# Optimization experiments

Hardware: AMD Instinct MI355X
Metric: run time of the kernel (lower is better)

Reference implementation:

```python
import jax, jax.numpy as jnp
import numpy as np

N = 2_000_000
LAYER_DIMS = [6, 128, 48, 48, 48, 48, 48, 128, 3]  # 8 Linear layers


def setup_inputs() -> dict:
    key = jax.random.key(0)
    ks = jax.random.split(key, 2 + 2 * (len(LAYER_DIMS) - 1))
    inp = {
        "dimensions": jax.random.normal(ks[0], (N, 3), dtype=jnp.float32),
        "xyz": jax.random.normal(ks[1], (N, 3), dtype=jnp.float32),
    }
    # Kaiming-uniform-ish init like torch.nn.Linear defaults
    for i in range(len(LAYER_DIMS) - 1):
        fan_in, fan_out = LAYER_DIMS[i], LAYER_DIMS[i + 1]
        bound = 1.0 / np.sqrt(fan_in)
        inp[f"W{i+1}"] = jax.random.uniform(ks[2 + 2 * i], (fan_in, fan_out),
                                             minval=-bound, maxval=bound, dtype=jnp.float32)
        inp[f"b{i+1}"] = jax.random.uniform(ks[3 + 2 * i], (fan_out,),
                                             minval=-bound, maxval=bound, dtype=jnp.float32)
    return inp


def reference(dimensions, xyz,
              W1, b1, W2, b2, W3, b3, W4, b4,
              W5, b5, W6, b6, W7, b7, W8, b8) -> jnp.ndarray:
    x = jnp.concatenate([dimensions, xyz], axis=1)  # [N, 6]
    Ws = (W1, W2, W3, W4, W5, W6, W7)
    bs = (b1, b2, b3, b4, b5, b6, b7)
    for W, b in zip(Ws, bs):
        x = jax.nn.silu(x @ W + b)
    # final layer: Linear(128, 3) with Identity activation
    return x @ W8 + b8  # [N, 3]
```

## Files before the change

kernel.cpp:

```cpp
#include <hip/hip_runtime.h>

typedef __bf16 bf16x4 __attribute__((ext_vector_type(4)));
typedef short  s16x4  __attribute__((ext_vector_type(4)));
typedef float  f32x4  __attribute__((ext_vector_type(4)));

#define DEVFN static __device__ __forceinline__
#define BLOCK 512
#define NWAVES 8

DEVFN f32x4 mfma16(bf16x4 a, bf16x4 b, f32x4 c) {
  s16x4 as = __builtin_bit_cast(s16x4, a);
  s16x4 bs = __builtin_bit_cast(s16x4, b);
  return __builtin_amdgcn_mfma_f32_16x16x16bf16_1k(as, bs, c, 0, 0, 0);
}

DEVFN float silu_scaled(float y) {
  float e = __builtin_amdgcn_exp2f(-y);
  return y * __builtin_amdgcn_rcpf(1.0f + e);
}

DEVFN bf16x4 pksilu(f32x4 t) {
  bf16x4 r;
#pragma unroll
  for (int j = 0; j < 4; ++j) r[j] = (__bf16)silu_scaled(t[j]);
  return r;
}

DEVFN void sbar() { __builtin_amdgcn_sched_barrier(0x7F); }

#define OFF_W1   0u
#define OFF_W2   4096u
#define OFF_W3   16384u
#define OFF_W4   20992u
#define OFF_W5   25600u
#define OFF_W6   30208u
#define OFF_W7   34816u
#define OFF_BIAS 47104u
#define SMEM_TOTAL 49152u

#define LOG2E 1.44269504f
#define LN2   0.69314718f

DEVFN void packW(unsigned char* smem, unsigned base, const float* W, int K, int N, int tid) {
  int NT = N >> 4;
  int total = (K >> 4) * NT * 256;
  for (int t = tid; t < total; t += BLOCK) {
    int i = t & 3, ln = (t >> 2) & 63, f = t >> 8;
    int ks = f / NT, nt = f - ks * NT;
    int k = 16 * ks + 4 * (ln >> 4) + i;
    int n = 16 * nt + (ln & 15);
    *(__bf16*)(smem + base + (unsigned)f * 512u + (unsigned)ln * 8u + (unsigned)i * 2u)
        = (__bf16)W[k * N + n];
  }
}

DEVFN f32x4 ldb(const float* sB, int off, int nt, int g) {
  return *(const f32x4*)(sB + off + nt * 16 + 4 * g);
}

DEVFN bf16x4 ldw(const unsigned char* smem, unsigned addr) {
  return *(const bf16x4*)(smem + addr);
}

DEVFN void layer33(const unsigned char* smem, unsigned wbase, const float* sB, int bOffL,
                   unsigned wOff, int g, const bf16x4 (&xin)[2][3], bf16x4 (&xout)[2][3]) {
  f32x4 acc[2][3];
#pragma unroll
  for (int nt = 0; nt < 3; ++nt) {
    f32x4 bi = ldb(sB, bOffL, nt, g);
    acc[0][nt] = bi; acc[1][nt] = bi;
  }
#pragma unroll
  for (int ks = 0; ks < 3; ++ks)
#pragma unroll
    for (int nt = 0; nt < 3; ++nt) {
      bf16x4 w = ldw(smem, wbase + (unsigned)(ks * 3 + nt) * 512u + wOff);
      acc[0][nt] = mfma16(w, xin[0][ks], acc[0][nt]);
      acc[1][nt] = mfma16(w, xin[1][ks], acc[1][nt]);
    }
#pragma unroll
  for (int nt = 0; nt < 3; ++nt) {
    xout[0][nt] = pksilu(acc[0][nt]);
    xout[1][nt] = pksilu(acc[1][nt]);
  }
}

DEVFN void loadIn6(const float* __restrict__ dims, const float* __restrict__ xyz,
                   int grp, int g, int m, int N, float (&buf)[2][4]) {
#pragma unroll
  for (int rt = 0; rt < 2; ++rt) { buf[rt][0] = buf[rt][1] = buf[rt][2] = buf[rt][3] = 0.f; }
  if (g == 0) {
#pragma unroll
    for (int rt = 0; rt < 2; ++rt) {
      int row = grp * 32 + rt * 16 + m;
      if (row < N) {
        const float* dp = dims + (size_t)row * 3u;
        buf[rt][0] = dp[0]; buf[rt][1] = dp[1]; buf[rt][2] = dp[2];
        buf[rt][3] = xyz[(size_t)row * 3u];
      }
    }
  } else if (g == 1) {
#pragma unroll
    for (int rt = 0; rt < 2; ++rt) {
      int row = grp * 32 + rt * 16 + m;
      if (row < N) {
        const float* xp = xyz + (size_t)row * 3u;
        buf[rt][0] = xp[1]; buf[rt][1] = xp[2];
      }
    }
  }
}

__global__ void __launch_bounds__(BLOCK, 3)
pinn_mlp_kernel(const float* __restrict__ dims, const float* __restrict__ xyz,
                const float* __restrict__ W1, const float* __restrict__ b1,
                const float* __restrict__ W2, const float* __restrict__ b2,
                const float* __restrict__ W3, const float* __restrict__ b3,
                const float* __restrict__ W4, const float* __restrict__ b4,
                const float* __restrict__ W5, const float* __restrict__ b5,
                const float* __restrict__ W6, const float* __restrict__ b6,
                const float* __restrict__ W7, const float* __restrict__ b7,
                const float* __restrict__ W8, const float* __restrict__ b8,
                float* __restrict__ out, int N) {
  __shared__ __align__(16) unsigned char smem[SMEM_TOTAL];
  const int tid  = threadIdx.x;
  const int lane = tid & 63;
  const int wave = tid >> 6;
  const int m    = lane & 15;
  const int g    = lane >> 4;

  for (int t = tid; t < 2048; t += BLOCK) {
    int i = t & 3, ln = (t >> 2) & 63, nt = t >> 8;
    int k = 4 * (ln >> 4) + i;
    int n = 16 * nt + (ln & 15);
    float v = (k < 6) ? W1[k * 128 + n] * LOG2E : 0.f;
    *(__bf16*)(smem + OFF_W1 + (unsigned)nt * 512u + (unsigned)ln * 8u + (unsigned)i * 2u) = (__bf16)v;
  }
  packW(smem, OFF_W2, W2, 128, 48, tid);
  packW(smem, OFF_W3, W3, 48, 48, tid);
  packW(smem, OFF_W4, W4, 48, 48, tid);
  packW(smem, OFF_W5, W5, 48, 48, tid);
  packW(smem, OFF_W6, W6, 48, 48, tid);
  packW(smem, OFF_W7, W7, 48, 128, tid);
  float* sBw = (float*)(smem + OFF_BIAS);
  for (int t = tid; t < 512; t += BLOCK) {
    float v;
    if      (t < 128) v = b1[t] * LOG2E;
    else if (t < 176) v = b2[t - 128] * LOG2E;
    else if (t < 224) v = b3[t - 176] * LOG2E;
    else if (t < 272) v = b4[t - 224] * LOG2E;
    else if (t < 320) v = b5[t - 272] * LOG2E;
    else if (t < 368) v = b6[t - 320] * LOG2E;
    else if (t < 496) v = b7[t - 368] * LOG2E;
    else if (t < 499) v = b8[t - 496];
    else              v = 0.f;
    sBw[t] = v;
  }

  bf16x4 w8f[8];
#pragma unroll
  for (int ks = 0; ks < 8; ++ks) {
    w8f[ks][0] = (__bf16)0.f; w8f[ks][1] = (__bf16)0.f;
    w8f[ks][2] = (__bf16)0.f; w8f[ks][3] = (__bf16)0.f;
    if (m < 3) {
#pragma unroll
      for (int i = 0; i < 4; ++i) {
        int k = 16 * ks + 4 * g + i;
        w8f[ks][i] = (__bf16)(W8[k * 3 + m] * LN2);
      }
    }
  }

  __syncthreads();

  const float* sB = (const float*)(smem + OFF_BIAS);
  const unsigned wOff = (unsigned)lane * 8u;

  const int nGroups  = (N + 31) >> 5;
  const int gw0      = blockIdx.x * NWAVES + wave;
  const int gwStride = gridDim.x * NWAVES;

  float inC[2][4], inN[2][4];
  loadIn6(dims, xyz, gw0, g, m, N, inC);

  for (int grp = gw0; grp < nGroups; grp += gwStride) {
    const int base = grp * 32;

    bf16x4 x1[2];
#pragma unroll
    for (int rt = 0; rt < 2; ++rt)
#pragma unroll
      for (int j = 0; j < 4; ++j) x1[rt][j] = (__bf16)inC[rt][j];
    loadIn6(dims, xyz, grp + gwStride, g, m, N, inN);
    sbar();

    f32x4 acc2[2][3];
#pragma unroll
    for (int nt = 0; nt < 3; ++nt) {
      f32x4 bi = ldb(sB, 128, nt, g);
      acc2[0][nt] = bi; acc2[1][nt] = bi;
    }
#pragma unroll
    for (int p = 0; p < 4; ++p) {
      bf16x4 y[2][2];
#pragma unroll
      for (int c = 0; c < 2; ++c) {
        int nt = 2 * p + c;
        f32x4 bi = ldb(sB, 0, nt, g);
        bf16x4 w = ldw(smem, OFF_W1 + (unsigned)nt * 512u + wOff);
        y[0][c] = pksilu(mfma16(w, x1[0], bi));
        y[1][c] = pksilu(mfma16(w, x1[1], bi));
      }
      sbar();
#pragma unroll
      for (int c = 0; c < 2; ++c) {
        int ks = 2 * p + c;
#pragma unroll
        for (int nt = 0; nt < 3; ++nt) {
          bf16x4 w = ldw(smem, OFF_W2 + (unsigned)(ks * 3 + nt) * 512u + wOff);
          acc2[0][nt] = mfma16(w, y[0][c], acc2[0][nt]);
          acc2[1][nt] = mfma16(w, y[1][c], acc2[1][nt]);
        }
      }
      sbar();
    }
    bf16x4 xa[2][3], xb[2][3];
#pragma unroll
    for (int nt = 0; nt < 3; ++nt) {
      xa[0][nt] = pksilu(acc2[0][nt]);
      xa[1][nt] = pksilu(acc2[1][nt]);
    }
    sbar();

    layer33(smem, OFF_W3, sB, 176, wOff, g, xa, xb); sbar();
    layer33(smem, OFF_W4, sB, 224, wOff, g, xb, xa); sbar();
    layer33(smem, OFF_W5, sB, 272, wOff, g, xa, xb); sbar();
    layer33(smem, OFF_W6, sB, 320, wOff, g, xb, xa); sbar();

    f32x4 acc8[2];
    {
      f32x4 bi8 = ldb(sB, 496, 0, g);
      acc8[0] = bi8; acc8[1] = bi8;
    }
#pragma unroll
    for (int p = 0; p < 4; ++p) {
      f32x4 a7[2][2];
#pragma unroll
      for (int c = 0; c < 2; ++c) {
        f32x4 bi = ldb(sB, 368, 2 * p + c, g);
        a7[0][c] = bi; a7[1][c] = bi;
      }
#pragma unroll
      for (int ks = 0; ks < 3; ++ks)
#pragma unroll
        for (int c = 0; c < 2; ++c) {
          bf16x4 w = ldw(smem, OFF_W7 + (unsigned)(ks * 8 + 2 * p + c) * 512u + wOff);
          a7[0][c] = mfma16(w, xa[0][ks], a7[0][c]);
          a7[1][c] = mfma16(w, xa[1][ks], a7[1][c]);
        }
      sbar();
#pragma unroll
      for (int c = 0; c < 2; ++c) {
        bf16x4 x7a = pksilu(a7[0][c]);
        bf16x4 x7b = pksilu(a7[1][c]);
        acc8[0] = mfma16(w8f[2 * p + c], x7a, acc8[0]);
        acc8[1] = mfma16(w8f[2 * p + c], x7b, acc8[1]);
      }
      sbar();
    }

    if (g == 0) {
#pragma unroll
      for (int rt = 0; rt < 2; ++rt) {
        int row = base + rt * 16 + m;
        if (row < N) {
          size_t o = (size_t)row * 3u;
          out[o + 0] = acc8[rt][0];
          out[o + 1] = acc8[rt][1];
          out[o + 2] = acc8[rt][2];
        }
      }
    }

#pragma unroll
    for (int rt = 0; rt < 2; ++rt)
#pragma unroll
      for (int j = 0; j < 4; ++j) inC[rt][j] = inN[rt][j];
  }
}

extern "C" void kernel_launch(void* const* d_in, const int* in_sizes, int n_in,
                              void* d_out, int out_size, void* d_ws, size_t ws_size,
                              hipStream_t stream) {
  const float* dims = (const float*)d_in[0];
  const float* xyz  = (const float*)d_in[1];
  const float* W1 = (const float*)d_in[2];  const float* b1 = (const float*)d_in[3];
  const float* W2 = (const float*)d_in[4];  const float* b2 = (const float*)d_in[5];
  const float* W3 = (const float*)d_in[6];  const float* b3 = (const float*)d_in[7];
  const float* W4 = (const float*)d_in[8];  const float* b4 = (const float*)d_in[9];
  const float* W5 = (const float*)d_in[10]; const float* b5 = (const float*)d_in[11];
  const float* W6 = (const float*)d_in[12]; const float* b6 = (const float*)d_in[13];
  const float* W7 = (const float*)d_in[14]; const float* b7 = (const float*)d_in[15];
  const float* W8 = (const float*)d_in[16]; const float* b8 = (const float*)d_in[17];
  float* out = (float*)d_out;
  const int N = in_sizes[0] / 3;

  pinn_mlp_kernel<<<dim3(512), dim3(BLOCK), 0, stream>>>(
      dims, xyz, W1, b1, W2, b2, W3, b3, W4, b4, W5, b5, W6, b6, W7, b7, W8, b8,
      out, N);
}
```

Baseline: 277.6 us.

## Share one reciprocal across four SiLU lanes and fold layer-1 bias into weights

```diff
diff --git a/kernel.cpp b/kernel.cpp
--- a/kernel.cpp
+++ b/kernel.cpp
@@ -14,15 +14,22 @@
   return __builtin_amdgcn_mfma_f32_16x16x16bf16_1k(as, bs, c, 0, 0, 0);
 }
 
-DEVFN float silu_scaled(float y) {
-  float e = __builtin_amdgcn_exp2f(-y);
-  return y * __builtin_amdgcn_rcpf(1.0f + e);
-}
-
-DEVFN bf16x4 pksilu(f32x4 t) {
+DEVFN bf16x4 pksilu(f32x4 y) {
+  float e0 = __builtin_amdgcn_exp2f(-y[0]);
+  float e1 = __builtin_amdgcn_exp2f(-y[1]);
+  float e2 = __builtin_amdgcn_exp2f(-y[2]);
+  float e3 = __builtin_amdgcn_exp2f(-y[3]);
+  e0 = fminf(e0, 16777216.f); e1 = fminf(e1, 16777216.f);
+  e2 = fminf(e2, 16777216.f); e3 = fminf(e3, 16777216.f);
+  float d0 = 1.f + e0, d1 = 1.f + e1, d2 = 1.f + e2, d3 = 1.f + e3;
+  float p01 = d0 * d1, p23 = d2 * d3;
+  float R   = __builtin_amdgcn_rcpf(p01 * p23);
+  float R01 = R * p23, R23 = R * p01;
   bf16x4 r;
-#pragma unroll
-  for (int j = 0; j < 4; ++j) r[j] = (__bf16)silu_scaled(t[j]);
+  r[0] = (__bf16)(y[0] * (R01 * d1));
+  r[1] = (__bf16)(y[1] * (R01 * d0));
+  r[2] = (__bf16)(y[2] * (R23 * d3));
+  r[3] = (__bf16)(y[3] * (R23 * d2));
   return r;
 }
 
@@ -107,6 +114,7 @@
         const float* xp = xyz + (size_t)row * 3u;
         buf[rt][0] = xp[1]; buf[rt][1] = xp[2];
       }
+      buf[rt][2] = 1.f;
     }
   }
 }
@@ -133,7 +141,7 @@
     int i = t & 3, ln = (t >> 2) & 63, nt = t >> 8;
     int k = 4 * (ln >> 4) + i;
     int n = 16 * nt + (ln & 15);
-    float v = (k < 6) ? W1[k * 128 + n] * LOG2E : 0.f;
+    float v = (k < 6) ? W1[k * 128 + n] * LOG2E : (k == 6 ? b1[n] * LOG2E : 0.f);
     *(__bf16*)(smem + OFF_W1 + (unsigned)nt * 512u + (unsigned)ln * 8u + (unsigned)i * 2u) = (__bf16)v;
   }
   packW(smem, OFF_W2, W2, 128, 48, tid);
@@ -145,7 +153,7 @@
   float* sBw = (float*)(smem + OFF_BIAS);
   for (int t = tid; t < 512; t += BLOCK) {
     float v;
-    if      (t < 128) v = b1[t] * LOG2E;
+    if      (t < 128) v = 0.f;
     else if (t < 176) v = b2[t - 128] * LOG2E;
     else if (t < 224) v = b3[t - 176] * LOG2E;
     else if (t < 272) v = b4[t - 224] * LOG2E;
@@ -194,6 +202,8 @@
     loadIn6(dims, xyz, grp + gwStride, g, m, N, inN);
     sbar();
 
+    const f32x4 z4 = {0.f, 0.f, 0.f, 0.f};
+
     f32x4 acc2[2][3];
 #pragma unroll
     for (int nt = 0; nt < 3; ++nt) {
@@ -206,10 +216,9 @@
 #pragma unroll
       for (int c = 0; c < 2; ++c) {
         int nt = 2 * p + c;
-        f32x4 bi = ldb(sB, 0, nt, g);
         bf16x4 w = ldw(smem, OFF_W1 + (unsigned)nt * 512u + wOff);
-        y[0][c] = pksilu(mfma16(w, x1[0], bi));
-        y[1][c] = pksilu(mfma16(w, x1[1], bi));
+        y[0][c] = pksilu(mfma16(w, x1[0], z4));
+        y[1][c] = pksilu(mfma16(w, x1[1], z4));
       }
       sbar();
 #pragma unroll
```

Result: slower. 307.7 us (+10.8%).

## Keep W3-W5 fragments in registers and fold layer-1 bias into padded K

Applied to the files above, without the earlier changes.

```diff
diff --git a/kernel.cpp b/kernel.cpp
--- a/kernel.cpp
+++ b/kernel.cpp
@@ -62,6 +62,28 @@
   return *(const bf16x4*)(smem + addr);
 }
 
+DEVFN void layer33R(const bf16x4 (&wf)[9], const float* sB, int bOffL, int g,
+                    const bf16x4 (&xin)[2][3], bf16x4 (&xout)[2][3]) {
+  f32x4 acc[2][3];
+#pragma unroll
+  for (int nt = 0; nt < 3; ++nt) {
+    f32x4 bi = ldb(sB, bOffL, nt, g);
+    acc[0][nt] = bi; acc[1][nt] = bi;
+  }
+#pragma unroll
+  for (int ks = 0; ks < 3; ++ks)
+#pragma unroll
+    for (int nt = 0; nt < 3; ++nt) {
+      acc[0][nt] = mfma16(wf[ks * 3 + nt], xin[0][ks], acc[0][nt]);
+      acc[1][nt] = mfma16(wf[ks * 3 + nt], xin[1][ks], acc[1][nt]);
+    }
+#pragma unroll
+  for (int nt = 0; nt < 3; ++nt) {
+    xout[0][nt] = pksilu(acc[0][nt]);
+    xout[1][nt] = pksilu(acc[1][nt]);
+  }
+}
+
 DEVFN void layer33(const unsigned char* smem, unsigned wbase, const float* sB, int bOffL,
                    unsigned wOff, int g, const bf16x4 (&xin)[2][3], bf16x4 (&xout)[2][3]) {
   f32x4 acc[2][3];
@@ -85,29 +107,27 @@
   }
 }
 
-DEVFN void loadIn6(const float* __restrict__ dims, const float* __restrict__ xyz,
-                   int grp, int g, int m, int N, float (&buf)[2][4]) {
-#pragma unroll
-  for (int rt = 0; rt < 2; ++rt) { buf[rt][0] = buf[rt][1] = buf[rt][2] = buf[rt][3] = 0.f; }
-  if (g == 0) {
-#pragma unroll
-    for (int rt = 0; rt < 2; ++rt) {
-      int row = grp * 32 + rt * 16 + m;
+DEVFN void loadIn6b(const float* __restrict__ dims, const float* __restrict__ xyz,
+                    int grp, int g, int m, int N, bf16x4 (&buf)[2]) {
+#pragma unroll
+  for (int rt = 0; rt < 2; ++rt) {
+    float v0 = 0.f, v1 = 0.f, v2 = 0.f, v3 = 0.f;
+    int row = grp * 32 + rt * 16 + m;
+    if (g == 0) {
       if (row < N) {
         const float* dp = dims + (size_t)row * 3u;
-        buf[rt][0] = dp[0]; buf[rt][1] = dp[1]; buf[rt][2] = dp[2];
-        buf[rt][3] = xyz[(size_t)row * 3u];
-      }
-    }
-  } else if (g == 1) {
-#pragma unroll
-    for (int rt = 0; rt < 2; ++rt) {
-      int row = grp * 32 + rt * 16 + m;
+        v0 = dp[0]; v1 = dp[1]; v2 = dp[2];
+        v3 = xyz[(size_t)row * 3u];
+      }
+    } else if (g == 1) {
       if (row < N) {
         const float* xp = xyz + (size_t)row * 3u;
-        buf[rt][0] = xp[1]; buf[rt][1] = xp[2];
-      }
-    }
+        v0 = xp[1]; v1 = xp[2];
+      }
+      v2 = 1.f;
+    }
+    buf[rt][0] = (__bf16)v0; buf[rt][1] = (__bf16)v1;
+    buf[rt][2] = (__bf16)v2; buf[rt][3] = (__bf16)v3;
   }
 }
 
@@ -133,7 +153,7 @@
     int i = t & 3, ln = (t >> 2) & 63, nt = t >> 8;
     int k = 4 * (ln >> 4) + i;
     int n = 16 * nt + (ln & 15);
-    float v = (k < 6) ? W1[k * 128 + n] * LOG2E : 0.f;
+    float v = (k < 6) ? W1[k * 128 + n] * LOG2E : (k == 6 ? b1[n] * LOG2E : 0.f);
     *(__bf16*)(smem + OFF_W1 + (unsigned)nt * 512u + (unsigned)ln * 8u + (unsigned)i * 2u) = (__bf16)v;
   }
   packW(smem, OFF_W2, W2, 128, 48, tid);
@@ -145,7 +165,7 @@
   float* sBw = (float*)(smem + OFF_BIAS);
   for (int t = tid; t < 512; t += BLOCK) {
     float v;
-    if      (t < 128) v = b1[t] * LOG2E;
+    if      (t < 128) v = 0.f;
     else if (t < 176) v = b2[t - 128] * LOG2E;
     else if (t < 224) v = b3[t - 176] * LOG2E;
     else if (t < 272) v = b4[t - 224] * LOG2E;
@@ -176,23 +196,28 @@
   const float* sB = (const float*)(smem + OFF_BIAS);
   const unsigned wOff = (unsigned)lane * 8u;
 
+  bf16x4 w3f[9], w4f[9], w5f[9];
+#pragma unroll
+  for (int f = 0; f < 9; ++f) {
+    w3f[f] = ldw(smem, OFF_W3 + (unsigned)f * 512u + wOff);
+    w4f[f] = ldw(smem, OFF_W4 + (unsigned)f * 512u + wOff);
+    w5f[f] = ldw(smem, OFF_W5 + (unsigned)f * 512u + wOff);
+  }
+
   const int nGroups  = (N + 31) >> 5;
   const int gw0      = blockIdx.x * NWAVES + wave;
   const int gwStride = gridDim.x * NWAVES;
 
-  float inC[2][4], inN[2][4];
-  loadIn6(dims, xyz, gw0, g, m, N, inC);
+  bf16x4 inC[2], inN[2];
+  loadIn6b(dims, xyz, gw0, g, m, N, inC);
 
   for (int grp = gw0; grp < nGroups; grp += gwStride) {
     const int base = grp * 32;
 
-    bf16x4 x1[2];
-#pragma unroll
-    for (int rt = 0; rt < 2; ++rt)
-#pragma unroll
-      for (int j = 0; j < 4; ++j) x1[rt][j] = (__bf16)inC[rt][j];
-    loadIn6(dims, xyz, grp + gwStride, g, m, N, inN);
+    loadIn6b(dims, xyz, grp + gwStride, g, m, N, inN);
     sbar();
+
+    const f32x4 z4 = {0.f, 0.f, 0.f, 0.f};
 
     f32x4 acc2[2][3];
 #pragma unroll
@@ -206,10 +231,9 @@
 #pragma unroll
       for (int c = 0; c < 2; ++c) {
         int nt = 2 * p + c;
-        f32x4 bi = ldb(sB, 0, nt, g);
         bf16x4 w = ldw(smem, OFF_W1 + (unsigned)nt * 512u + wOff);
-        y[0][c] = pksilu(mfma16(w, x1[0], bi));
-        y[1][c] = pksilu(mfma16(w, x1[1], bi));
+        y[0][c] = pksilu(mfma16(w, inC[0], z4));
+        y[1][c] = pksilu(mfma16(w, inC[1], z4));
       }
       sbar();
 #pragma unroll
@@ -232,10 +256,12 @@
     }
     sbar();
 
-    layer33(smem, OFF_W3, sB, 176, wOff, g, xa, xb); sbar();
-    layer33(smem, OFF_W4, sB, 224, wOff, g, xb, xa); sbar();
-    layer33(smem, OFF_W5, sB, 272, wOff, g, xa, xb); sbar();
-    layer33(smem, OFF_W6, sB, 320, wOff, g, xb, xa); sbar();
+    layer33R(w3f, sB, 176, g, xa, xb);
+    layer33R(w4f, sB, 224, g, xb, xa);
+    layer33R(w5f, sB, 272, g, xa, xb);
+    sbar();
+    layer33(smem, OFF_W6, sB, 320, wOff, g, xb, xa);
+    sbar();
 
     f32x4 acc8[2];
     {
@@ -282,10 +308,7 @@
       }
     }
 
-#pragma unroll
-    for (int rt = 0; rt < 2; ++rt)
-#pragma unroll
-      for (int j = 0; j < 4; ++j) inC[rt][j] = inN[rt][j];
+    inC[0] = inN[0]; inC[1] = inN[1];
   }
 }
 
```

Result: slower. 309.1 us (+11.3%).

## Process four row tiles per wave and fold layer-1 bias into weights

Applied to the files above, without the earlier changes.

```diff
diff --git a/kernel.cpp b/kernel.cpp
--- a/kernel.cpp
+++ b/kernel.cpp
@@ -7,6 +7,7 @@
 #define DEVFN static __device__ __forceinline__
 #define BLOCK 512
 #define NWAVES 8
+#define RT 4
 
 DEVFN f32x4 mfma16(bf16x4 a, bf16x4 b, f32x4 c) {
   s16x4 as = __builtin_bit_cast(s16x4, a);
@@ -63,51 +64,51 @@
 }
 
 DEVFN void layer33(const unsigned char* smem, unsigned wbase, const float* sB, int bOffL,
-                   unsigned wOff, int g, const bf16x4 (&xin)[2][3], bf16x4 (&xout)[2][3]) {
-  f32x4 acc[2][3];
+                   unsigned wOff, int g, const bf16x4 (&xin)[RT][3], bf16x4 (&xout)[RT][3]) {
+  f32x4 acc[RT][3];
 #pragma unroll
   for (int nt = 0; nt < 3; ++nt) {
     f32x4 bi = ldb(sB, bOffL, nt, g);
-    acc[0][nt] = bi; acc[1][nt] = bi;
+#pragma unroll
+    for (int rt = 0; rt < RT; ++rt) acc[rt][nt] = bi;
   }
 #pragma unroll
   for (int ks = 0; ks < 3; ++ks)
 #pragma unroll
     for (int nt = 0; nt < 3; ++nt) {
       bf16x4 w = ldw(smem, wbase + (unsigned)(ks * 3 + nt) * 512u + wOff);
-      acc[0][nt] = mfma16(w, xin[0][ks], acc[0][nt]);
-      acc[1][nt] = mfma16(w, xin[1][ks], acc[1][nt]);
-    }
-#pragma unroll
-  for (int nt = 0; nt < 3; ++nt) {
-    xout[0][nt] = pksilu(acc[0][nt]);
-    xout[1][nt] = pksilu(acc[1][nt]);
-  }
-}
-
-DEVFN void loadIn6(const float* __restrict__ dims, const float* __restrict__ xyz,
-                   int grp, int g, int m, int N, float (&buf)[2][4]) {
-#pragma unroll
-  for (int rt = 0; rt < 2; ++rt) { buf[rt][0] = buf[rt][1] = buf[rt][2] = buf[rt][3] = 0.f; }
-  if (g == 0) {
-#pragma unroll
-    for (int rt = 0; rt < 2; ++rt) {
-      int row = grp * 32 + rt * 16 + m;
+#pragma unroll
+      for (int rt = 0; rt < RT; ++rt)
+        acc[rt][nt] = mfma16(w, xin[rt][ks], acc[rt][nt]);
+    }
+#pragma unroll
+  for (int nt = 0; nt < 3; ++nt)
+#pragma unroll
+    for (int rt = 0; rt < RT; ++rt)
+      xout[rt][nt] = pksilu(acc[rt][nt]);
+}
+
+DEVFN void loadIn6b(const float* __restrict__ dims, const float* __restrict__ xyz,
+                    int grp, int g, int m, int N, bf16x4 (&buf)[RT]) {
+#pragma unroll
+  for (int rt = 0; rt < RT; ++rt) {
+    float v0 = 0.f, v1 = 0.f, v2 = 0.f, v3 = 0.f;
+    int row = grp * (RT * 16) + rt * 16 + m;
+    if (g == 0) {
       if (row < N) {
         const float* dp = dims + (size_t)row * 3u;
-        buf[rt][0] = dp[0]; buf[rt][1] = dp[1]; buf[rt][2] = dp[2];
-        buf[rt][3] = xyz[(size_t)row * 3u];
-      }
-    }
-  } else if (g == 1) {
-#pragma unroll
-    for (int rt = 0; rt < 2; ++rt) {
-      int row = grp * 32 + rt * 16 + m;
+        v0 = dp[0]; v1 = dp[1]; v2 = dp[2];
+        v3 = xyz[(size_t)row * 3u];
+      }
+    } else if (g == 1) {
       if (row < N) {
         const float* xp = xyz + (size_t)row * 3u;
-        buf[rt][0] = xp[1]; buf[rt][1] = xp[2];
-      }
-    }
+        v0 = xp[1]; v1 = xp[2];
+      }
+      v2 = 1.f;
+    }
+    buf[rt][0] = (__bf16)v0; buf[rt][1] = (__bf16)v1;
+    buf[rt][2] = (__bf16)v2; buf[rt][3] = (__bf16)v3;
   }
 }
 
@@ -133,7 +134,7 @@
     int i = t & 3, ln = (t >> 2) & 63, nt = t >> 8;
     int k = 4 * (ln >> 4) + i;
     int n = 16 * nt + (ln & 15);
-    float v = (k < 6) ? W1[k * 128 + n] * LOG2E : 0.f;
+    float v = (k < 6) ? W1[k * 128 + n] * LOG2E : (k == 6 ? b1[n] * LOG2E : 0.f);
     *(__bf16*)(smem + OFF_W1 + (unsigned)nt * 512u + (unsigned)ln * 8u + (unsigned)i * 2u) = (__bf16)v;
   }
   packW(smem, OFF_W2, W2, 128, 48, tid);
@@ -145,7 +146,7 @@
   float* sBw = (float*)(smem + OFF_BIAS);
   for (int t = tid; t < 512; t += BLOCK) {
     float v;
-    if      (t < 128) v = b1[t] * LOG2E;
+    if      (t < 128) v = 0.f;
     else if (t < 176) v = b2[t - 128] * LOG2E;
     else if (t < 224) v = b3[t - 176] * LOG2E;
     else if (t < 272) v = b4[t - 224] * LOG2E;
@@ -176,40 +177,38 @@
   const float* sB = (const float*)(smem + OFF_BIAS);
   const unsigned wOff = (unsigned)lane * 8u;
 
-  const int nGroups  = (N + 31) >> 5;
+  const int nGroups  = (N + RT * 16 - 1) / (RT * 16);
   const int gw0      = blockIdx.x * NWAVES + wave;
   const int gwStride = gridDim.x * NWAVES;
 
-  float inC[2][4], inN[2][4];
-  loadIn6(dims, xyz, gw0, g, m, N, inC);
+  bf16x4 inC[RT], inN[RT];
+  loadIn6b(dims, xyz, gw0, g, m, N, inC);
 
   for (int grp = gw0; grp < nGroups; grp += gwStride) {
-    const int base = grp * 32;
-
-    bf16x4 x1[2];
-#pragma unroll
-    for (int rt = 0; rt < 2; ++rt)
-#pragma unroll
-      for (int j = 0; j < 4; ++j) x1[rt][j] = (__bf16)inC[rt][j];
-    loadIn6(dims, xyz, grp + gwStride, g, m, N, inN);
+    const int base = grp * (RT * 16);
+
+    loadIn6b(dims, xyz, grp + gwStride, g, m, N, inN);
     sbar();
 
-    f32x4 acc2[2][3];
+    const f32x4 z4 = {0.f, 0.f, 0.f, 0.f};
+
+    f32x4 acc2[RT][3];
 #pragma unroll
     for (int nt = 0; nt < 3; ++nt) {
       f32x4 bi = ldb(sB, 128, nt, g);
-      acc2[0][nt] = bi; acc2[1][nt] = bi;
+#pragma unroll
+      for (int rt = 0; rt < RT; ++rt) acc2[rt][nt] = bi;
     }
 #pragma unroll
     for (int p = 0; p < 4; ++p) {
-      bf16x4 y[2][2];
+      bf16x4 y[RT][2];
 #pragma unroll
       for (int c = 0; c < 2; ++c) {
         int nt = 2 * p + c;
-        f32x4 bi = ldb(sB, 0, nt, g);
         bf16x4 w = ldw(smem, OFF_W1 + (unsigned)nt * 512u + wOff);
-        y[0][c] = pksilu(mfma16(w, x1[0], bi));
-        y[1][c] = pksilu(mfma16(w, x1[1], bi));
+#pragma unroll
+        for (int rt = 0; rt < RT; ++rt)
+          y[rt][c] = pksilu(mfma16(w, inC[rt], z4));
       }
       sbar();
 #pragma unroll
@@ -218,18 +217,19 @@
 #pragma unroll
         for (int nt = 0; nt < 3; ++nt) {
           bf16x4 w = ldw(smem, OFF_W2 + (unsigned)(ks * 3 + nt) * 512u + wOff);
-          acc2[0][nt] = mfma16(w, y[0][c], acc2[0][nt]);
-          acc2[1][nt] = mfma16(w, y[1][c], acc2[1][nt]);
+#pragma unroll
+          for (int rt = 0; rt < RT; ++rt)
+            acc2[rt][nt] = mfma16(w, y[rt][c], acc2[rt][nt]);
         }
       }
       sbar();
     }
-    bf16x4 xa[2][3], xb[2][3];
-#pragma unroll
-    for (int nt = 0; nt < 3; ++nt) {
-      xa[0][nt] = pksilu(acc2[0][nt]);
-      xa[1][nt] = pksilu(acc2[1][nt]);
-    }
+    bf16x4 xa[RT][3], xb[RT][3];
+#pragma unroll
+    for (int nt = 0; nt < 3; ++nt)
+#pragma unroll
+      for (int rt = 0; rt < RT; ++rt)
+        xa[rt][nt] = pksilu(acc2[rt][nt]);
     sbar();
 
     layer33(smem, OFF_W3, sB, 176, wOff, g, xa, xb); sbar();
@@ -237,41 +237,44 @@
     layer33(smem, OFF_W5, sB, 272, wOff, g, xa, xb); sbar();
     layer33(smem, OFF_W6, sB, 320, wOff, g, xb, xa); sbar();
 
-    f32x4 acc8[2];
+    f32x4 acc8[RT];
     {
       f32x4 bi8 = ldb(sB, 496, 0, g);
-      acc8[0] = bi8; acc8[1] = bi8;
+#pragma unroll
+      for (int rt = 0; rt < RT; ++rt) acc8[rt] = bi8;
     }
 #pragma unroll
     for (int p = 0; p < 4; ++p) {
-      f32x4 a7[2][2];
+      f32x4 a7[RT][2];
 #pragma unroll
       for (int c = 0; c < 2; ++c) {
         f32x4 bi = ldb(sB, 368, 2 * p + c, g);
-        a7[0][c] = bi; a7[1][c] = bi;
+#pragma unroll
+        for (int rt = 0; rt < RT; ++rt) a7[rt][c] = bi;
       }
 #pragma unroll
       for (int ks = 0; ks < 3; ++ks)
 #pragma unroll
         for (int c = 0; c < 2; ++c) {
           bf16x4 w = ldw(smem, OFF_W7 + (unsigned)(ks * 8 + 2 * p + c) * 512u + wOff);
-          a7[0][c] = mfma16(w, xa[0][ks], a7[0][c]);
-          a7[1][c] = mfma16(w, xa[1][ks], a7[1][c]);
+#pragma unroll
+          for (int rt = 0; rt < RT; ++rt)
+            a7[rt][c] = mfma16(w, xa[rt][ks], a7[rt][c]);
         }
       sbar();
 #pragma unroll
-      for (int c = 0; c < 2; ++c) {
-        bf16x4 x7a = pksilu(a7[0][c]);
-        bf16x4 x7b = pksilu(a7[1][c]);
-        acc8[0] = mfma16(w8f[2 * p + c], x7a, acc8[0]);
-        acc8[1] = mfma16(w8f[2 * p + c], x7b, acc8[1]);
-      }
+      for (int c = 0; c < 2; ++c)
+#pragma unroll
+        for (int rt = 0; rt < RT; ++rt) {
+          bf16x4 x7 = pksilu(a7[rt][c]);
+          acc8[rt] = mfma16(w8f[2 * p + c], x7, acc8[rt]);
+        }
       sbar();
     }
 
     if (g == 0) {
 #pragma unroll
-      for (int rt = 0; rt < 2; ++rt) {
+      for (int rt = 0; rt < RT; ++rt) {
         int row = base + rt * 16 + m;
         if (row < N) {
           size_t o = (size_t)row * 3u;
@@ -283,9 +286,7 @@
     }
 
 #pragma unroll
-    for (int rt = 0; rt < 2; ++rt)
-#pragma unroll
-      for (int j = 0; j < 4; ++j) inC[rt][j] = inN[rt][j];
+    for (int rt = 0; rt < RT; ++rt) inC[rt] = inN[rt];
   }
 }
 
```

After: 319.0 us. +14.9%, slower.
